# Optimization experiments

Measured on AMD Instinct MI355X. Metric: run time of the kernel, lower is better.

## Reference

```python
import jax, jax.numpy as jnp
import numpy as np

N_NODES = 50000
N_EDGES = 500000


def setup_inputs() -> dict:
    key = jax.random.key(0)
    ks = jax.random.split(key, 24)
    p = {}
    p['x_feat'] = jax.random.normal(ks[0], (N_NODES, 24), dtype=jnp.float32)
    p['edge_index'] = jax.random.randint(ks[1], (2, N_EDGES), 0, N_NODES)
    p['edge_attr'] = jax.random.uniform(ks[2], (N_EDGES, 16), dtype=jnp.float32)
    def lin(k, fan_in, shape):
        b = 1.0 / np.sqrt(fan_in)
        return jax.random.uniform(k, shape, jnp.float32, -b, b)
    # group-0 input projection: 24 -> 32
    p['lin_prep_W'] = lin(ks[3], 24, (24, 32)); p['lin_prep_b'] = lin(ks[4], 24, (32,))
    # prep tube: 32 -> 16
    p['tube_W'] = lin(ks[5], 32, (32, 16)); p['tube_b'] = lin(ks[6], 32, (16,))
    # shared edge-attr trunk: 16 -> 32 -> 16
    p['edge_W1'] = lin(ks[7], 16, (16, 32)); p['edge_b1'] = lin(ks[8], 16, (32,))
    p['edge_W2'] = lin(ks[9], 32, (32, 16)); p['edge_b2'] = lin(ks[10], 32, (16,))
    # conv1: in=16, out=8 per aggr (mean, max, add)
    p['conv1_edge_W'] = lin(ks[11], 16, (3, 16, 16 * 8)); p['conv1_edge_b'] = lin(ks[12], 16, (3, 16 * 8))
    p['conv1_root_W'] = lin(ks[13], 16, (3, 16, 8)); p['conv1_bias'] = lin(ks[14], 16, (3, 8))
    # conv2: in=24, out=8 per aggr
    p['conv2_edge_W'] = lin(ks[15], 16, (3, 16, 24 * 8)); p['conv2_edge_b'] = lin(ks[16], 16, (3, 24 * 8))
    p['conv2_root_W'] = lin(ks[17], 24, (3, 24, 8)); p['conv2_bias'] = lin(ks[18], 24, (3, 8))
    # output head: 24 -> 2
    p['out_W'] = lin(ks[19], 24, (24, 2)); p['out_b'] = lin(ks[20], 24, (2,))
    return p


def _nnconv(x, e_repr, src, dst, edge_W, edge_b, root_W, bias, n_nodes):
    # x: [N, in]; e_repr: [E, 16]; edge_W: [3, 16, in*out]
    d_in = x.shape[1]
    x_src = x[src]  # [E, in]
    deg = jax.ops.segment_sum(jnp.ones_like(src, dtype=x.dtype), dst, num_segments=n_nodes)  # [N]
    outs = []
    for a, aggr in enumerate(('mean', 'max', 'add')):
        W_e = (e_repr @ edge_W[a] + edge_b[a]).reshape(e_repr.shape[0], d_in, -1)  # [E, in, out]
        msg = jnp.einsum('ei,eio->eo', x_src, W_e)  # [E, out]
        if aggr == 'add':
            agg = jax.ops.segment_sum(msg, dst, num_segments=n_nodes)
        elif aggr == 'mean':
            agg = jax.ops.segment_sum(msg, dst, num_segments=n_nodes) / jnp.maximum(deg, 1.0)[:, None]
        else:
            agg = jax.ops.segment_max(msg, dst, num_segments=n_nodes)
            agg = jnp.where(deg[:, None] > 0, agg, 0.0)  # no-neighbor nodes -> 0
        outs.append(agg + x @ root_W[a] + bias[a])
    return jax.nn.relu(jnp.concatenate(outs, axis=1))  # [N, 3*out]


def reference(x_feat, edge_index, edge_attr, lin_prep_W, lin_prep_b, tube_W, tube_b,
              edge_W1, edge_b1, edge_W2, edge_b2,
              conv1_edge_W, conv1_edge_b, conv1_root_W, conv1_bias,
              conv2_edge_W, conv2_edge_b, conv2_root_W, conv2_bias,
              out_W, out_b):
    n_nodes = x_feat.shape[0]
    src, dst = edge_index[0], edge_index[1]
    # node prep: group projection + tube (relu acts, dropout=0 -> identity)
    x = jax.nn.relu(x_feat @ lin_prep_W + lin_prep_b)       # [N, 32]
    x = jax.nn.relu(x @ tube_W + tube_b)                    # [N, 16]
    # shared edge-attr trunk (last activation = sigmoid), computed once
    e = jax.nn.relu(edge_attr @ edge_W1 + edge_b1)
    e_repr = jax.nn.sigmoid(e @ edge_W2 + edge_b2)          # [E, 16]
    # hop 1 and hop 2 of edge-conditioned NNConv with mean/max/add aggregators
    x = _nnconv(x, e_repr, src, dst, conv1_edge_W, conv1_edge_b, conv1_root_W, conv1_bias, n_nodes)  # [N, 24]
    x = _nnconv(x, e_repr, src, dst, conv2_edge_W, conv2_edge_b, conv2_root_W, conv2_bias, n_nodes)  # [N, 24]
    logits = x @ out_W + out_b                              # [N, 2]
    scores = jax.nn.softmax(logits, axis=1)
    return (logits, scores)
```

## Files before the change

### kernel.cpp

```cpp
#include <hip/hip_runtime.h>

#define BS 256

__device__ __forceinline__ unsigned short f2bf(float f) {
    unsigned x = __float_as_uint(f);
    return (unsigned short)((x + 0x7fffu + ((x >> 16) & 1u)) >> 16);
}
__device__ __forceinline__ unsigned pack2bf(float a, float b) {
    return (unsigned)f2bf(a) | ((unsigned)f2bf(b) << 16);
}
__device__ __forceinline__ void unpack2(unsigned u, float* d) {
    d[0] = __uint_as_float(u << 16);
    d[1] = __uint_as_float(u & 0xFFFF0000u);
}
__device__ __forceinline__ void unpack8(uint4 v, float* d) {
    unpack2(v.x, d); unpack2(v.y, d + 2); unpack2(v.z, d + 4); unpack2(v.w, d + 6);
}
__device__ __forceinline__ uint4 pack8bf(const float* r) {
    return make_uint4(pack2bf(r[0], r[1]), pack2bf(r[2], r[3]),
                      pack2bf(r[4], r[5]), pack2bf(r[6], r[7]));
}

__global__ void prep_kernel(const float* __restrict__ xf,
                            const float* __restrict__ W1, const float* __restrict__ b1,
                            const float* __restrict__ W2, const float* __restrict__ b2,
                            float* __restrict__ x16, int N)
{
    int n = blockIdx.x * blockDim.x + threadIdx.x;
    bool valid = n < N;
    int nn = valid ? n : 0;
    float a[24];
#pragma unroll
    for (int i = 0; i < 24; i += 4)
        *(float4*)(a + i) = *(const float4*)(xf + (size_t)nn * 24 + i);
    float h[32];
#pragma unroll
    for (int j = 0; j < 32; j++) {
        float s = b1[j];
#pragma unroll
        for (int i = 0; i < 24; i++) s = fmaf(a[i], W1[i * 32 + j], s);
        h[j] = fmaxf(s, 0.f);
    }
    if (!valid) return;
#pragma unroll
    for (int j = 0; j < 16; j++) {
        float s = b2[j];
#pragma unroll
        for (int i = 0; i < 32; i++) s = fmaf(h[i], W2[i * 16 + j], s);
        x16[(size_t)n * 16 + j] = fmaxf(s, 0.f);
    }
}

__global__ void degjj_kernel(const int* __restrict__ srcA, const int* __restrict__ dstA,
                             int* __restrict__ cntS, int* __restrict__ cntD,
                             int* __restrict__ jS, int* __restrict__ jD, int E)
{
    int base = blockIdx.x * (BS * 4) + threadIdx.x;
    int e0 = base, e1 = base + BS, e2 = base + 2 * BS, e3 = base + 3 * BS;
    bool v0 = e0 < E, v1 = e1 < E, v2 = e2 < E, v3 = e3 < E;
    int s0 = 0, s1 = 0, s2 = 0, s3 = 0, d0 = 0, d1 = 0, d2 = 0, d3 = 0;
    if (v0) { s0 = srcA[e0]; d0 = dstA[e0]; }
    if (v1) { s1 = srcA[e1]; d1 = dstA[e1]; }
    if (v2) { s2 = srcA[e2]; d2 = dstA[e2]; }
    if (v3) { s3 = srcA[e3]; d3 = dstA[e3]; }
    int a0 = 0, a1 = 0, a2 = 0, a3 = 0, b0 = 0, b1 = 0, b2 = 0, b3 = 0;
    if (v0) { a0 = atomicAdd(&cntS[s0], 1); b0 = atomicAdd(&cntD[d0], 1); }
    if (v1) { a1 = atomicAdd(&cntS[s1], 1); b1 = atomicAdd(&cntD[d1], 1); }
    if (v2) { a2 = atomicAdd(&cntS[s2], 1); b2 = atomicAdd(&cntD[d2], 1); }
    if (v3) { a3 = atomicAdd(&cntS[s3], 1); b3 = atomicAdd(&cntD[d3], 1); }
    if (v0) { jS[e0] = a0; jD[e0] = b0; }
    if (v1) { jS[e1] = a1; jD[e1] = b1; }
    if (v2) { jS[e2] = a2; jD[e2] = b2; }
    if (v3) { jS[e3] = a3; jD[e3] = b3; }
}

__global__ void offsets2_kernel(const int* __restrict__ cntS, const int* __restrict__ cntD,
                                int* __restrict__ offsS, int* __restrict__ offsD,
                                int* __restrict__ cursS, int* __restrict__ cursD, int N)
{
    int n = blockIdx.x * blockDim.x + threadIdx.x;
    int lane = threadIdx.x & 63;
    bool valid = n < N;
    int dS = valid ? cntS[n] : 0;
    int dD = valid ? cntD[n] : 0;
    int sS = dS, sD = dD;
#pragma unroll
    for (int o = 1; o < 64; o <<= 1) {
        int tS = __shfl_up(sS, o);
        int tD = __shfl_up(sD, o);
        if (lane >= o) { sS += tS; sD += tD; }
    }
    int totS = __shfl(sS, 63);
    int totD = __shfl(sD, 63);
    int baseS = 0, baseD = 0;
    if (lane == 63) {
        baseS = atomicAdd(cursS, totS);
        baseD = atomicAdd(cursD, totD);
    }
    baseS = __shfl(baseS, 63);
    baseD = __shfl(baseD, 63);
    if (valid) {
        offsS[n] = baseS + sS - dS;
        offsD[n] = baseD + sD - dD;
    }
}

__global__ __launch_bounds__(BS) void er_fill_kernel(
    const int* __restrict__ srcA, const int* __restrict__ dstA,
    const int* __restrict__ jS, const int* __restrict__ jD,
    const int* __restrict__ offsS, const int* __restrict__ offsD,
    const float* __restrict__ eattr,
    const float* __restrict__ eW1, const float* __restrict__ eb1,
    const float* __restrict__ eW2, const float* __restrict__ eb2,
    uint4* __restrict__ erec, int E)
{
    int e = blockIdx.x * BS + threadIdx.x;
    if (e >= E) return;
    int s = srcA[e], d = dstA[e];
    int p = offsS[s] + jS[e];
    int q = offsD[d] + jD[e];

    float ea[16];
#pragma unroll
    for (int i = 0; i < 16; i += 4)
        *(float4*)(ea + i) = *(const float4*)(eattr + (size_t)e * 16 + i);
    float h[32];
#pragma unroll
    for (int j = 0; j < 32; j++) {
        float t = eb1[j];
#pragma unroll
        for (int i = 0; i < 16; i++) t = fmaf(ea[i], eW1[i * 32 + j], t);
        h[j] = fmaxf(t, 0.f);
    }
    float er[16];
#pragma unroll
    for (int j = 0; j < 16; j++) {
        float t = eb2[j];
#pragma unroll
        for (int i = 0; i < 32; i++) t = fmaf(h[i], eW2[i * 16 + j], t);
        er[j] = 1.f / (1.f + __expf(-t));
    }
    unsigned w[8];
#pragma unroll
    for (int j = 0; j < 8; j++) w[j] = pack2bf(er[2 * j], er[2 * j + 1]);
    uint4* rp = erec + (size_t)p * 4;
    rp[0] = make_uint4((unsigned)s, (unsigned)q, w[0], w[1]);
    rp[1] = make_uint4(w[2], w[3], w[4], w[5]);
    rp[2] = make_uint4(w[6], w[7], 0u, 0u);
    rp[3] = make_uint4(0u, 0u, 0u, 0u);
}

template <int IN>
__global__ __launch_bounds__(BS) void ynode_kernel(const float* __restrict__ x,
                                                   const float* __restrict__ W,
                                                   const float* __restrict__ B,
                                                   const float* __restrict__ RW,
                                                   const float* __restrict__ RB,
                                                   unsigned short* __restrict__ Y,
                                                   float* __restrict__ root, int N)
{
    __shared__ float4 w4[IN * 6];
    __shared__ unsigned outb[512 * 13];
    int t = threadIdx.x;
    int k = blockIdx.y;

    for (int idx = t; idx < IN * 6; idx += BS) {
        int i = idx / 6;
        int c = idx - i * 6;
        int a = c >> 1;
        int o = (c & 1) * 4;
        const float* srcp;
        if (k < 16)       srcp = W + (((size_t)a * 16 + k) * IN + i) * 8 + o;
        else if (k == 16) srcp = B + ((size_t)a * IN + i) * 8 + o;
        else              srcp = RW + ((size_t)a * IN + i) * 8 + o;
        w4[idx] = *(const float4*)srcp;
    }
    __syncthreads();

    int nbase = blockIdx.x * (BS * 2);
    int n0 = nbase + t;
    int n1 = n0 + BS;
    bool v0 = n0 < N, v1 = n1 < N;
    int m0 = v0 ? n0 : 0, m1 = v1 ? n1 : 0;

    float xa[IN], xb[IN];
#pragma unroll
    for (int i = 0; i < IN; i += 4) {
        *(float4*)(xa + i) = *(const float4*)(x + (size_t)m0 * IN + i);
        *(float4*)(xb + i) = *(const float4*)(x + (size_t)m1 * IN + i);
    }

    float ra[24], rb[24];
#pragma unroll
    for (int j = 0; j < 24; j++) { ra[j] = 0.f; rb[j] = 0.f; }

#pragma unroll
    for (int i = 0; i < IN; i++) {
        float x0 = xa[i], x1 = xb[i];
#pragma unroll
        for (int c = 0; c < 6; c++) {
            float4 w = w4[i * 6 + c];
            ra[c*4+0] = fmaf(x0, w.x, ra[c*4+0]); ra[c*4+1] = fmaf(x0, w.y, ra[c*4+1]);
            ra[c*4+2] = fmaf(x0, w.z, ra[c*4+2]); ra[c*4+3] = fmaf(x0, w.w, ra[c*4+3]);
            rb[c*4+0] = fmaf(x1, w.x, rb[c*4+0]); rb[c*4+1] = fmaf(x1, w.y, rb[c*4+1]);
            rb[c*4+2] = fmaf(x1, w.z, rb[c*4+2]); rb[c*4+3] = fmaf(x1, w.w, rb[c*4+3]);
        }
    }

    if (k < 17) {
#pragma unroll
        for (int j = 0; j < 12; j++) {
            outb[t * 13 + j] = pack2bf(ra[2 * j], ra[2 * j + 1]);
            outb[(t + BS) * 13 + j] = pack2bf(rb[2 * j], rb[2 * j + 1]);
        }
        __syncthreads();
        unsigned* gbase = (unsigned*)(Y + ((size_t)k * N + nbase) * 24);
        int rows = N - nbase; if (rows > 512) rows = 512;
        if (rows == 512) {
#pragma unroll
            for (int v = 0; v < 6; v++) {
                int g = (v * BS + t) * 4;
                uint4 val;
                val.x = outb[((g + 0) / 12) * 13 + (g + 0) % 12];
                val.y = outb[((g + 1) / 12) * 13 + (g + 1) % 12];
                val.z = outb[((g + 2) / 12) * 13 + (g + 2) % 12];
                val.w = outb[((g + 3) / 12) * 13 + (g + 3) % 12];
                *(uint4*)(gbase + g) = val;
            }
        } else {
            int totU = rows * 12;
            for (int g = t; g < totU; g += BS)
                gbase[g] = outb[(g / 12) * 13 + g % 12];
        }
    } else {
        if (v0) {
            float* pr = root + (size_t)n0 * 24;
#pragma unroll
            for (int j = 0; j < 24; j += 4)
                *(float4*)(pr + j) = make_float4(ra[j] + RB[j], ra[j+1] + RB[j+1],
                                                 ra[j+2] + RB[j+2], ra[j+3] + RB[j+3]);
        }
        if (v1) {
            float* pr = root + (size_t)n1 * 24;
#pragma unroll
            for (int j = 0; j < 24; j += 4)
                *(float4*)(pr + j) = make_float4(rb[j] + RB[j], rb[j+1] + RB[j+1],
                                                 rb[j+2] + RB[j+2], rb[j+3] + RB[j+3]);
        }
    }
}

__global__ __launch_bounds__(BS) void msg_kernel(
    const uint4* __restrict__ erec,
    const unsigned short* __restrict__ Y,
    unsigned short* __restrict__ msg16,
    int N, int E)
{
    int tid = blockIdx.x * BS + threadIdx.x;
    int p = tid / 3;
    int j = tid - p * 3;
    if (p >= E) return;

    const uint4* rp = erec + (size_t)p * 4;
    uint4 r0 = rp[0];
    uint4 r1 = rp[1];
    uint4 r2 = rp[2];
    unsigned s = r0.x, q = r0.y;

    float er[16];
    unpack2(r0.z, er); unpack2(r0.w, er + 2);
    unpack8(r1, er + 4);
    unpack2(r2.x, er + 12); unpack2(r2.y, er + 14);

    const unsigned short* yb = Y + (size_t)s * 24 + j * 8;
    size_t kstride = (size_t)N * 24;

    float acc[8];
    unpack8(*(const uint4*)(yb + 16 * kstride), acc);
#pragma unroll
    for (int k = 0; k < 16; k++) {
        float t[8];
        unpack8(*(const uint4*)(yb + (size_t)k * kstride), t);
        float ek = er[k];
#pragma unroll
        for (int o = 0; o < 8; o++) acc[o] = fmaf(ek, t[o], acc[o]);
    }
    unsigned short* mrow = msg16 + (size_t)q * 32;
    *(uint4*)(mrow + j * 8) = pack8bf(acc);
    if (j == 0) *(uint4*)(mrow + 24) = make_uint4(0, 0, 0, 0);
}

__global__ __launch_bounds__(BS) void gather_kernel(
    const unsigned short* __restrict__ msg16,
    const int* __restrict__ offs,
    const int* __restrict__ degi,
    const float* __restrict__ root,
    float* __restrict__ out, int N)
{
    int n = (blockIdx.x * BS + threadIdx.x) >> 6;
    if (n >= N) return;
    int lane = threadIdx.x & 63;
    int c = lane & 3;
    int r = lane >> 2;

    int off = offs[n];
    int d = degi[n];

    float s[8], m[8];
#pragma unroll
    for (int o = 0; o < 8; o++) { s[o] = 0.f; m[o] = -3.402823466e38f; }

    if (c < 3) {
        const unsigned short* base = msg16 + (size_t)off * 32 + c * 8;
        for (int j = r; j < d; j += 16) {
            uint4 v = *(const uint4*)(base + (size_t)j * 32);
            float t[8];
            unpack8(v, t);
#pragma unroll
            for (int o = 0; o < 8; o++) {
                s[o] += t[o];
                m[o] = fmaxf(m[o], t[o]);
            }
        }
    }
#pragma unroll
    for (int mask = 4; mask < 64; mask <<= 1) {
#pragma unroll
        for (int o = 0; o < 8; o++) {
            s[o] += __shfl_xor(s[o], mask);
            m[o] = fmaxf(m[o], __shfl_xor(m[o], mask));
        }
    }
    if (lane >= 3) return;

    float inv = 1.f / fmaxf((float)d, 1.f);
    const float* pr = root + (size_t)n * 24 + c * 8;
    float4 r0 = *(const float4*)(pr);
    float4 r1 = *(const float4*)(pr + 4);
    float rb[8] = {r0.x, r0.y, r0.z, r0.w, r1.x, r1.y, r1.z, r1.w};
    float rr[8];
#pragma unroll
    for (int o = 0; o < 8; o++) {
        float agg = (c == 0) ? s[o] * inv
                  : (c == 1) ? ((d > 0) ? m[o] : 0.f)
                  : s[o];
        rr[o] = fmaxf(rb[o] + agg, 0.f);
    }
    float* po = out + (size_t)n * 24 + c * 8;
    *(float4*)(po)     = make_float4(rr[0], rr[1], rr[2], rr[3]);
    *(float4*)(po + 4) = make_float4(rr[4], rr[5], rr[6], rr[7]);
}

__global__ void head_kernel(const float* __restrict__ x, const float* __restrict__ W,
                            const float* __restrict__ b, float* __restrict__ out, int N)
{
    int n = blockIdx.x * blockDim.x + threadIdx.x;
    if (n >= N) return;
    float l0 = b[0], l1 = b[1];
#pragma unroll
    for (int i = 0; i < 24; i++) {
        float xi = x[(size_t)n * 24 + i];
        l0 = fmaf(xi, W[i * 2 + 0], l0);
        l1 = fmaf(xi, W[i * 2 + 1], l1);
    }
    out[2 * (size_t)n + 0] = l0;
    out[2 * (size_t)n + 1] = l1;
    float mx = fmaxf(l0, l1);
    float e0 = __expf(l0 - mx), e1 = __expf(l1 - mx);
    float sm = e0 + e1;
    out[2 * (size_t)N + 2 * (size_t)n + 0] = e0 / sm;
    out[2 * (size_t)N + 2 * (size_t)n + 1] = e1 / sm;
}

extern "C" void kernel_launch(void* const* d_in, const int* in_sizes, int n_in,
                              void* d_out, int out_size, void* d_ws, size_t ws_size,
                              hipStream_t stream)
{
    const float* x_feat = (const float*)d_in[0];
    const int*   eidx   = (const int*)d_in[1];
    const float* eattr  = (const float*)d_in[2];
    const float* lpW = (const float*)d_in[3];
    const float* lpb = (const float*)d_in[4];
    const float* tW  = (const float*)d_in[5];
    const float* tb  = (const float*)d_in[6];
    const float* eW1 = (const float*)d_in[7];
    const float* eb1 = (const float*)d_in[8];
    const float* eW2 = (const float*)d_in[9];
    const float* eb2 = (const float*)d_in[10];
    const float* c1W = (const float*)d_in[11];
    const float* c1B = (const float*)d_in[12];
    const float* c1R = (const float*)d_in[13];
    const float* c1b = (const float*)d_in[14];
    const float* c2W = (const float*)d_in[15];
    const float* c2B = (const float*)d_in[16];
    const float* c2R = (const float*)d_in[17];
    const float* c2b = (const float*)d_in[18];
    const float* oW  = (const float*)d_in[19];
    const float* ob  = (const float*)d_in[20];

    int N = in_sizes[0] / 24;
    int E = in_sizes[1] / 2;
    const int* srcA = eidx;
    const int* dstA = eidx + E;

    char* wsb = (char*)d_ws;
    size_t off = 0;
    auto alloc = [&](size_t bytes) {
        off = (off + 255) & ~(size_t)255;
        void* p = wsb + off;
        off += bytes;
        return p;
    };
    unsigned short* Y     = (unsigned short*)alloc((size_t)17 * N * 24 * 2);
    unsigned short* msg16 = (unsigned short*)alloc((size_t)E * 32 * 2);
    uint4* erec = (uint4*)alloc((size_t)E * 64);
    float* root = (float*)alloc((size_t)N * 24 * 4);
    float* x16  = (float*)alloc((size_t)N * 16 * 4);
    float* x24a = (float*)alloc((size_t)N * 24 * 4);
    float* x24b = (float*)alloc((size_t)N * 24 * 4);
    int* ibase  = (int*)alloc(((size_t)2 * N + 2) * 4);
    int* cntS = ibase;
    int* cntD = ibase + N;
    int* cursS = ibase + 2 * N;
    int* cursD = ibase + 2 * N + 1;
    int* offsS = (int*)alloc((size_t)N * 4);
    int* offsD = (int*)alloc((size_t)N * 4);
    int* jS    = (int*)alloc((size_t)E * 4);
    int* jD    = (int*)alloc((size_t)E * 4);

    dim3 blk(BS);
    int nb_nodes = (N + BS - 1) / BS;
    int nb_edges = (E + BS - 1) / BS;
    int nb_deg   = (E + BS * 4 - 1) / (BS * 4);
    int nb_msg   = (3 * E + BS - 1) / BS;
    int nb_gath  = ((size_t)N * 64 + BS - 1) / BS;
    int nb_ypair = (N + BS * 2 - 1) / (BS * 2);
    dim3 ygrid(nb_ypair, 18);

    hipMemsetAsync(ibase, 0, (2 * (size_t)N + 2) * 4, stream);

    prep_kernel<<<nb_nodes, blk, 0, stream>>>(x_feat, lpW, lpb, tW, tb, x16, N);

    degjj_kernel<<<nb_deg, blk, 0, stream>>>(srcA, dstA, cntS, cntD, jS, jD, E);
    offsets2_kernel<<<nb_nodes, blk, 0, stream>>>(cntS, cntD, offsS, offsD, cursS, cursD, N);
    er_fill_kernel<<<nb_edges, blk, 0, stream>>>(srcA, dstA, jS, jD, offsS, offsD,
                                                 eattr, eW1, eb1, eW2, eb2, erec, E);

    ynode_kernel<16><<<ygrid, blk, 0, stream>>>(x16, c1W, c1B, c1R, c1b, Y, root, N);
    msg_kernel<<<nb_msg, blk, 0, stream>>>(erec, Y, msg16, N, E);
    gather_kernel<<<nb_gath, blk, 0, stream>>>(msg16, offsD, cntD, root, x24a, N);

    ynode_kernel<24><<<ygrid, blk, 0, stream>>>(x24a, c2W, c2B, c2R, c2b, Y, root, N);
    msg_kernel<<<nb_msg, blk, 0, stream>>>(erec, Y, msg16, N, E);
    gather_kernel<<<nb_gath, blk, 0, stream>>>(msg16, offsD, cntD, root, x24b, N);

    head_kernel<<<nb_nodes, blk, 0, stream>>>(x24b, oW, ob, (float*)d_out, N);
}
```

Measured before the change: 284.6 us.

## Split ynode work to one thread per node-aggregator with direct stores

Restructures the per-node weight-projection kernel so each thread computes one aggregator's 8 outputs for a single node, instead of all 24 outputs for two nodes. The LDS staging buffer and transposed coalesced store path are dropped; each thread writes its 8 bf16 outputs (16 bytes) or 8 floats straight to global memory. This gives smaller register footprint, more threads and a simpler store path, but each node's x row is now read three times and global stores are less coalesced.

```diff
diff --git a/kernel.cpp b/kernel.cpp
--- a/kernel.cpp
+++ b/kernel.cpp
@@ -159,94 +159,52 @@
                                                    unsigned short* __restrict__ Y,
                                                    float* __restrict__ root, int N)
 {
-    __shared__ float4 w4[IN * 6];
-    __shared__ unsigned outb[512 * 13];
+    __shared__ float w_lds[IN * 24];
     int t = threadIdx.x;
     int k = blockIdx.y;
 
-    for (int idx = t; idx < IN * 6; idx += BS) {
-        int i = idx / 6;
-        int c = idx - i * 6;
-        int a = c >> 1;
-        int o = (c & 1) * 4;
-        const float* srcp;
-        if (k < 16)       srcp = W + (((size_t)a * 16 + k) * IN + i) * 8 + o;
-        else if (k == 16) srcp = B + ((size_t)a * IN + i) * 8 + o;
-        else              srcp = RW + ((size_t)a * IN + i) * 8 + o;
-        w4[idx] = *(const float4*)srcp;
+    for (int idx = t; idx < IN * 24; idx += BS) {
+        int i = idx / 24;
+        int j = idx - i * 24;
+        int a = j >> 3, o = j & 7;
+        float v;
+        if (k < 16)       v = W[(((size_t)a * 16 + k) * IN + i) * 8 + o];
+        else if (k == 16) v = B[((size_t)a * IN + i) * 8 + o];
+        else              v = RW[((size_t)a * IN + i) * 8 + o];
+        w_lds[idx] = v;
     }
     __syncthreads();
 
-    int nbase = blockIdx.x * (BS * 2);
-    int n0 = nbase + t;
-    int n1 = n0 + BS;
-    bool v0 = n0 < N, v1 = n1 < N;
-    int m0 = v0 ? n0 : 0, m1 = v1 ? n1 : 0;
-
-    float xa[IN], xb[IN];
-#pragma unroll
-    for (int i = 0; i < IN; i += 4) {
-        *(float4*)(xa + i) = *(const float4*)(x + (size_t)m0 * IN + i);
-        *(float4*)(xb + i) = *(const float4*)(x + (size_t)m1 * IN + i);
-    }
-
-    float ra[24], rb[24];
-#pragma unroll
-    for (int j = 0; j < 24; j++) { ra[j] = 0.f; rb[j] = 0.f; }
-
+    int tid = blockIdx.x * BS + t;
+    int n = tid / 3;
+    int a = tid - n * 3;
+    if (n >= N) return;
+
+    float xv[IN];
+#pragma unroll
+    for (int i = 0; i < IN; i += 4)
+        *(float4*)(xv + i) = *(const float4*)(x + (size_t)n * IN + i);
+
+    float acc[8];
+#pragma unroll
+    for (int o = 0; o < 8; o++) acc[o] = 0.f;
+    const float* wb = w_lds + a * 8;
 #pragma unroll
     for (int i = 0; i < IN; i++) {
-        float x0 = xa[i], x1 = xb[i];
-#pragma unroll
-        for (int c = 0; c < 6; c++) {
-            float4 w = w4[i * 6 + c];
-            ra[c*4+0] = fmaf(x0, w.x, ra[c*4+0]); ra[c*4+1] = fmaf(x0, w.y, ra[c*4+1]);
-            ra[c*4+2] = fmaf(x0, w.z, ra[c*4+2]); ra[c*4+3] = fmaf(x0, w.w, ra[c*4+3]);
-            rb[c*4+0] = fmaf(x1, w.x, rb[c*4+0]); rb[c*4+1] = fmaf(x1, w.y, rb[c*4+1]);
-            rb[c*4+2] = fmaf(x1, w.z, rb[c*4+2]); rb[c*4+3] = fmaf(x1, w.w, rb[c*4+3]);
-        }
+        float xi = xv[i];
+#pragma unroll
+        for (int o = 0; o < 8; o++)
+            acc[o] = fmaf(xi, wb[i * 24 + o], acc[o]);
     }
 
     if (k < 17) {
-#pragma unroll
-        for (int j = 0; j < 12; j++) {
-            outb[t * 13 + j] = pack2bf(ra[2 * j], ra[2 * j + 1]);
-            outb[(t + BS) * 13 + j] = pack2bf(rb[2 * j], rb[2 * j + 1]);
-        }
-        __syncthreads();
-        unsigned* gbase = (unsigned*)(Y + ((size_t)k * N + nbase) * 24);
-        int rows = N - nbase; if (rows > 512) rows = 512;
-        if (rows == 512) {
-#pragma unroll
-            for (int v = 0; v < 6; v++) {
-                int g = (v * BS + t) * 4;
-                uint4 val;
-                val.x = outb[((g + 0) / 12) * 13 + (g + 0) % 12];
-                val.y = outb[((g + 1) / 12) * 13 + (g + 1) % 12];
-                val.z = outb[((g + 2) / 12) * 13 + (g + 2) % 12];
-                val.w = outb[((g + 3) / 12) * 13 + (g + 3) % 12];
-                *(uint4*)(gbase + g) = val;
-            }
-        } else {
-            int totU = rows * 12;
-            for (int g = t; g < totU; g += BS)
-                gbase[g] = outb[(g / 12) * 13 + g % 12];
-        }
+        *(uint4*)(Y + ((size_t)k * N + n) * 24 + a * 8) = pack8bf(acc);
     } else {
-        if (v0) {
-            float* pr = root + (size_t)n0 * 24;
-#pragma unroll
-            for (int j = 0; j < 24; j += 4)
-                *(float4*)(pr + j) = make_float4(ra[j] + RB[j], ra[j+1] + RB[j+1],
-                                                 ra[j+2] + RB[j+2], ra[j+3] + RB[j+3]);
-        }
-        if (v1) {
-            float* pr = root + (size_t)n1 * 24;
-#pragma unroll
-            for (int j = 0; j < 24; j += 4)
-                *(float4*)(pr + j) = make_float4(rb[j] + RB[j], rb[j+1] + RB[j+1],
-                                                 rb[j+2] + RB[j+2], rb[j+3] + RB[j+3]);
-        }
+        float* pr = root + (size_t)n * 24 + a * 8;
+        *(float4*)(pr)     = make_float4(acc[0] + RB[a*8+0], acc[1] + RB[a*8+1],
+                                         acc[2] + RB[a*8+2], acc[3] + RB[a*8+3]);
+        *(float4*)(pr + 4) = make_float4(acc[4] + RB[a*8+4], acc[5] + RB[a*8+5],
+                                         acc[6] + RB[a*8+6], acc[7] + RB[a*8+7]);
     }
 }
 
@@ -434,8 +392,8 @@
     int nb_deg   = (E + BS * 4 - 1) / (BS * 4);
     int nb_msg   = (3 * E + BS - 1) / BS;
     int nb_gath  = ((size_t)N * 64 + BS - 1) / BS;
-    int nb_ypair = (N + BS * 2 - 1) / (BS * 2);
-    dim3 ygrid(nb_ypair, 18);
+    int nb_y3    = (3 * N + BS - 1) / BS;
+    dim3 ygrid(nb_y3, 18);
 
     hipMemsetAsync(ibase, 0, (2 * (size_t)N + 2) * 4, stream);
 
```

Result: no change. 284.9 us (+0.1%).
